# Optimization experiments

Measured on AMD Instinct MI355X. Metric: run time of the kernel, lower is better.

The kernel has to match this reference:

```python
import jax, jax.numpy as jnp
import numpy as np

N_NODES = 100000


def gcn_conv(x, edge_src, edge_dst, edge_weight, W, b):
    # support = x @ W ; out = A @ support + b  (A given as weighted edge list)
    h = x @ W                                   # [N, d_out]
    msg = h[edge_src] * edge_weight[:, None]     # [E, d_out]
    agg = jax.ops.segment_sum(msg, edge_dst, num_segments=N_NODES)
    return agg + b


def setup_inputs() -> dict:
    key = jax.random.key(0)
    ks = jax.random.split(key, 8)
    N, E, m, hidden, m_y = N_NODES, 1600000, 128, 64, 32
    x = jax.random.normal(ks[0], (N, m), dtype=jnp.float32)
    edge_src = jax.random.randint(ks[1], (E,), 0, N, dtype=jnp.int32)
    edge_dst = jax.random.randint(ks[2], (E,), 0, N, dtype=jnp.int32)
    edge_weight = jax.random.uniform(ks[3], (E,), dtype=jnp.float32)
    s1 = 1.0 / np.sqrt(m)
    s2 = 1.0 / np.sqrt(hidden)
    W1 = jax.random.uniform(ks[4], (m, hidden), dtype=jnp.float32, minval=-s1, maxval=s1)
    b1 = jax.random.uniform(ks[5], (hidden,), dtype=jnp.float32, minval=-s1, maxval=s1)
    W2 = jax.random.uniform(ks[6], (hidden, m_y), dtype=jnp.float32, minval=-s2, maxval=s2)
    b2 = jax.random.uniform(ks[7], (m_y,), dtype=jnp.float32, minval=-s2, maxval=s2)
    return {"x": x, "edge_src": edge_src, "edge_dst": edge_dst,
            "edge_weight": edge_weight, "W1": W1, "b1": b1, "W2": W2, "b2": b2}


def reference(x, edge_src, edge_dst, edge_weight, W1, b1, W2, b2):
    out = gcn_conv(x, edge_src, edge_dst, edge_weight, W1, b1)
    out = jax.nn.relu(out)
    # F.dropout(p=0.5, training=self.training) -> identity in eval mode
    out = gcn_conv(out, edge_src, edge_dst, edge_weight, W2, b2)
    return out
```

## Files before the change

kernel.cpp:

```cpp
#include <hip/hip_runtime.h>
#include <hip/hip_bf16.h>


typedef unsigned short u16;
typedef unsigned int uint;
typedef short short8 __attribute__((ext_vector_type(8)));
typedef float floatx4 __attribute__((ext_vector_type(4)));

static __device__ __forceinline__ u16 f2bf(float f) {
    unsigned int u = __float_as_uint(f);
    return (u16)((u + 0x7fff + ((u >> 16) & 1)) >> 16);
}

#define F4C(v, j) ((j)==0?(v).x:((j)==1?(v).y:((j)==2?(v).z:(v).w)))
#define CHUNK 2048
#define CAPC 4608
#define ECAP 384

__global__ __launch_bounds__(256) void init_kernel(
    const float* __restrict__ W1, u16* __restrict__ wfg, int* __restrict__ gcursor)
{
    const int idx = blockIdx.x * 256 + threadIdx.x;
    if (idx < 512) gcursor[idx] = 0;
    const float4 v = ((const float4*)W1)[idx];
    const int k = idx >> 4, n4 = (idx & 15) * 4;
    const int step = k >> 5, klane = (k >> 3) & 3, j = k & 7;
    #pragma unroll
    for (int c = 0; c < 4; c++) {
        int n = n4 + c;
        wfg[(((n >> 4) * 4 + step) * 64 + klane * 16 + (n & 15)) * 8 + j] = f2bf(F4C(v, c));
    }
}

union __align__(16) SharedU {
    struct {
        u16 xs[64][136];
        u16 wf[4][4][64][8];
    } g;
    struct {
        int2 stage[CHUNK];
        u16  stb[CHUNK];
        int  hist[512], sc[512], xscan[512], place[512], runbase[512];
    } p;
};

__global__ __launch_bounds__(256, 4) void g1p_kernel(
    const float* __restrict__ x, const u16* __restrict__ wfg,
    u16* __restrict__ h1, int N,
    const int* __restrict__ src, const int* __restrict__ dst,
    const float* __restrict__ w, int* __restrict__ gcursor,
    int2* __restrict__ es, int E, int cap, int pblocks)
{
    __shared__ SharedU sh;
    const int tid = threadIdx.x;

    if (blockIdx.x < pblocks) {
        const int base = blockIdx.x * CHUNK;
        const int nloc = min(CHUNK, E - base);

        sh.p.hist[tid] = 0; sh.p.hist[tid + 256] = 0;
        __syncthreads();
        for (int i = tid; i < nloc; i += 256)
            atomicAdd(&sh.p.hist[dst[base + i] >> 8], 1);
        __syncthreads();

        sh.p.sc[tid] = sh.p.hist[tid];
        sh.p.sc[tid + 256] = sh.p.hist[tid + 256];
        __syncthreads();
        for (int o = 1; o < 512; o <<= 1) {
            int v0 = (tid >= o) ? sh.p.sc[tid - o] : 0;
            int v1 = (tid + 256 >= o) ? sh.p.sc[tid + 256 - o] : 0;
            __syncthreads();
            sh.p.sc[tid] += v0;
            sh.p.sc[tid + 256] += v1;
            __syncthreads();
        }
        sh.p.xscan[tid] = sh.p.sc[tid] - sh.p.hist[tid];
        sh.p.xscan[tid + 256] = sh.p.sc[tid + 256] - sh.p.hist[tid + 256];
        sh.p.place[tid] = sh.p.xscan[tid];
        sh.p.place[tid + 256] = sh.p.xscan[tid + 256];
        __syncthreads();

        for (int i = tid; i < nloc; i += 256) {
            int d = dst[base + i];
            int b = d >> 8;
            int pos = atomicAdd(&sh.p.place[b], 1);
            sh.p.stage[pos] = make_int2(src[base + i] | ((d & 255) << 24),
                                        __float_as_int(w[base + i]));
            sh.p.stb[pos] = (u16)b;
        }
        __syncthreads();

        {
            int l0 = sh.p.hist[tid], l1 = sh.p.hist[tid + 256];
            sh.p.runbase[tid]       = l0 ? atomicAdd(&gcursor[tid], l0)       : 0;
            sh.p.runbase[tid + 256] = l1 ? atomicAdd(&gcursor[tid + 256], l1) : 0;
        }
        __syncthreads();

        for (int i = tid; i < nloc; i += 256) {
            int b = sh.p.stb[i];
            es[(size_t)b * cap + sh.p.runbase[b] + (i - sh.p.xscan[b])] = sh.p.stage[i];
        }
        return;
    }

    const int row0 = (blockIdx.x - pblocks) * 64;
    {
        const float4* wg4 = (const float4*)wfg;
        float4* wl4 = (float4*)&sh.g.wf[0][0][0][0];
        #pragma unroll
        for (int i = 0; i < 4; i++) wl4[tid + i*256] = wg4[tid + i*256];
    }
    {
        const float4* x4 = (const float4*)x;
        #pragma unroll
        for (int i = 0; i < 8; i++) {
            int idx = tid + i*256;
            int r = idx >> 5, kc = idx & 31;
            int gr = row0 + r;
            float4 v = make_float4(0.f,0.f,0.f,0.f);
            if (gr < N) v = x4[gr*32 + kc];
            ushort4 o;
            o.x = f2bf(v.x); o.y = f2bf(v.y); o.z = f2bf(v.z); o.w = f2bf(v.w);
            *(ushort4*)&sh.g.xs[r][kc*4] = o;
        }
    }
    __syncthreads();

    const int wave = tid >> 6, lane = tid & 63;
    const int m = lane & 15, quad = lane >> 4;
    const int rw = wave * 16;

    floatx4 acc[4] = {(floatx4)(0.f), (floatx4)(0.f), (floatx4)(0.f), (floatx4)(0.f)};
    #pragma unroll
    for (int step = 0; step < 4; step++) {
        short8 a = *(const short8*)&sh.g.xs[rw + m][step*32 + quad*8];
        #pragma unroll
        for (int nt = 0; nt < 4; nt++) {
            short8 b = *(const short8*)&sh.g.wf[nt][step][lane][0];
            acc[nt] = __builtin_amdgcn_mfma_f32_16x16x32_bf16(a, b, acc[nt], 0, 0, 0);
        }
    }
    #pragma unroll
    for (int nt = 0; nt < 4; nt++) {
        #pragma unroll
        for (int r = 0; r < 4; r++) {
            int gr = row0 + rw + quad*4 + r;
            if (gr < N) h1[(size_t)gr*64 + nt*16 + m] = f2bf(acc[nt][r]);
        }
    }
}

__global__ __launch_bounds__(512, 4) void sg1_kernel(
    const u16* __restrict__ h1, const int2* __restrict__ es,
    const int* __restrict__ gcursor, int2* __restrict__ es2,
    int2* __restrict__ off2, const float* __restrict__ b1,
    const float* __restrict__ W2, u16* __restrict__ h2, int N, int cap)
{
    __shared__ int2 sorted[CAPC];
    __shared__ __align__(16) u16 ts[8][16][72];
    __shared__ __align__(16) u16 wf2[2][2][64][8];
    __shared__ float b1s[64];
    __shared__ int hist[256], exs[256], cur[256];
    const int t = threadIdx.x;
    const int b = blockIdx.x;
    const int e0 = b * cap;
    const int len = min(gcursor[b], CAPC);

    {
        const float4* s4 = (const float4*)W2;
        float4 v = s4[t];
        int k = t >> 3, n4 = (t & 7) * 4;
        int step = k >> 5, quad = (k >> 3) & 3, j = k & 7;
        #pragma unroll
        for (int c = 0; c < 4; c++) {
            int n = n4 + c;
            wf2[n >> 4][step][quad*16 + (n & 15)][j] = f2bf(F4C(v, c));
        }
        if (t < 16) ((float4*)b1s)[t] = ((const float4*)b1)[t];
        if (t < 256) hist[t] = 0;
    }
    __syncthreads();

    int2 re[9]; int rk[9];
    #pragma unroll
    for (int k = 0; k < 9; k++) {
        int i = t + k * 512;
        if (i < len) {
            re[k] = es[e0 + i];
            rk[k] = (int)(((unsigned)re[k].x) >> 24);
            atomicAdd(&hist[rk[k]], 1);
        } else rk[k] = -1;
    }
    __syncthreads();

    int v = 0;
    if (t < 256) { v = hist[t]; cur[t] = v; }
    __syncthreads();
    for (int o = 1; o < 256; o <<= 1) {
        int add = 0;
        if (t < 256 && t >= o) add = cur[t - o];
        __syncthreads();
        if (t < 256) cur[t] += add;
        __syncthreads();
    }
    if (t < 256) {
        int ex = cur[t] - v;
        exs[t] = ex;
        cur[t] = ex;
        int g = b * 256 + t;
        if (g < N) off2[g] = make_int2(e0 + ex, e0 + ex + v);
    }
    __syncthreads();

    #pragma unroll
    for (int k = 0; k < 9; k++)
        if (rk[k] >= 0) sorted[atomicAdd(&cur[rk[k]], 1)] = re[k];
    __syncthreads();

    for (int i = t; i < len; i += 512)
        es2[e0 + i] = sorted[i];

    const int wave = t >> 6, lane = t & 63;
    const int h = lane >> 4, fl = lane & 15;
    const uint2* h1v = (const uint2*)h1;
    uint* tsu = (uint*)&ts[wave][0][0];

    #pragma unroll 1
    for (int half = 0; half < 2; half++) {
        const int n0 = wave * 32 + half * 16;
        #pragma unroll 1
        for (int j = 0; j < 8; j++) {
            const int nA = n0 + j, nB = n0 + j + 8;
            const int pbegA = exs[nA], pendA = pbegA + hist[nA];
            const int pbegB = exs[nB], pendB = pbegB + hist[nB];
            const int clA = max(pendA - 1, 0), clB = max(pendB - 1, 0);
            float a0 = 0.f, a1 = 0.f, a2 = 0.f, a3 = 0.f;
            float c0 = 0.f, c1 = 0.f, c2 = 0.f, c3 = 0.f;
            int pA = pbegA, pB = pbegB;
            #pragma unroll 1
            while (pA < pendA || pB < pendB) {
                const int iA0 = pA + h,     iA1 = pA + 4 + h;
                const int iA2 = pA + 8 + h, iA3 = pA + 12 + h;
                const int iB0 = pB + h,     iB1 = pB + 4 + h;
                const int iB2 = pB + 8 + h, iB3 = pB + 12 + h;
                int2 eA0 = sorted[min(iA0, clA)];
                int2 eA1 = sorted[min(iA1, clA)];
                int2 eA2 = sorted[min(iA2, clA)];
                int2 eA3 = sorted[min(iA3, clA)];
                int2 eB0 = sorted[min(iB0, clB)];
                int2 eB1 = sorted[min(iB1, clB)];
                int2 eB2 = sorted[min(iB2, clB)];
                int2 eB3 = sorted[min(iB3, clB)];
                uint2 vA0 = h1v[(size_t)(eA0.x & 0xFFFFFF) * 16 + fl];
                uint2 vA1 = h1v[(size_t)(eA1.x & 0xFFFFFF) * 16 + fl];
                uint2 vA2 = h1v[(size_t)(eA2.x & 0xFFFFFF) * 16 + fl];
                uint2 vA3 = h1v[(size_t)(eA3.x & 0xFFFFFF) * 16 + fl];
                uint2 vB0 = h1v[(size_t)(eB0.x & 0xFFFFFF) * 16 + fl];
                uint2 vB1 = h1v[(size_t)(eB1.x & 0xFFFFFF) * 16 + fl];
                uint2 vB2 = h1v[(size_t)(eB2.x & 0xFFFFFF) * 16 + fl];
                uint2 vB3 = h1v[(size_t)(eB3.x & 0xFFFFFF) * 16 + fl];
                float wA0 = (iA0 < pendA) ? __int_as_float(eA0.y) : 0.f;
                float wA1 = (iA1 < pendA) ? __int_as_float(eA1.y) : 0.f;
                float wA2 = (iA2 < pendA) ? __int_as_float(eA2.y) : 0.f;
                float wA3 = (iA3 < pendA) ? __int_as_float(eA3.y) : 0.f;
                float wB0 = (iB0 < pendB) ? __int_as_float(eB0.y) : 0.f;
                float wB1 = (iB1 < pendB) ? __int_as_float(eB1.y) : 0.f;
                float wB2 = (iB2 < pendB) ? __int_as_float(eB2.y) : 0.f;
                float wB3 = (iB3 < pendB) ? __int_as_float(eB3.y) : 0.f;
                a0 += __uint_as_float(vA0.x << 16) * wA0 + __uint_as_float(vA1.x << 16) * wA1
                    + __uint_as_float(vA2.x << 16) * wA2 + __uint_as_float(vA3.x << 16) * wA3;
                a1 += __uint_as_float(vA0.x & 0xFFFF0000u) * wA0 + __uint_as_float(vA1.x & 0xFFFF0000u) * wA1
                    + __uint_as_float(vA2.x & 0xFFFF0000u) * wA2 + __uint_as_float(vA3.x & 0xFFFF0000u) * wA3;
                a2 += __uint_as_float(vA0.y << 16) * wA0 + __uint_as_float(vA1.y << 16) * wA1
                    + __uint_as_float(vA2.y << 16) * wA2 + __uint_as_float(vA3.y << 16) * wA3;
                a3 += __uint_as_float(vA0.y & 0xFFFF0000u) * wA0 + __uint_as_float(vA1.y & 0xFFFF0000u) * wA1
                    + __uint_as_float(vA2.y & 0xFFFF0000u) * wA2 + __uint_as_float(vA3.y & 0xFFFF0000u) * wA3;
                c0 += __uint_as_float(vB0.x << 16) * wB0 + __uint_as_float(vB1.x << 16) * wB1
                    + __uint_as_float(vB2.x << 16) * wB2 + __uint_as_float(vB3.x << 16) * wB3;
                c1 += __uint_as_float(vB0.x & 0xFFFF0000u) * wB0 + __uint_as_float(vB1.x & 0xFFFF0000u) * wB1
                    + __uint_as_float(vB2.x & 0xFFFF0000u) * wB2 + __uint_as_float(vB3.x & 0xFFFF0000u) * wB3;
                c2 += __uint_as_float(vB0.y << 16) * wB0 + __uint_as_float(vB1.y << 16) * wB1
                    + __uint_as_float(vB2.y << 16) * wB2 + __uint_as_float(vB3.y << 16) * wB3;
                c3 += __uint_as_float(vB0.y & 0xFFFF0000u) * wB0 + __uint_as_float(vB1.y & 0xFFFF0000u) * wB1
                    + __uint_as_float(vB2.y & 0xFFFF0000u) * wB2 + __uint_as_float(vB3.y & 0xFFFF0000u) * wB3;
                pA += 16; pB += 16;
            }
            a0 += __shfl_xor(a0, 16, 64); a1 += __shfl_xor(a1, 16, 64);
            a2 += __shfl_xor(a2, 16, 64); a3 += __shfl_xor(a3, 16, 64);
            a0 += __shfl_xor(a0, 32, 64); a1 += __shfl_xor(a1, 32, 64);
            a2 += __shfl_xor(a2, 32, 64); a3 += __shfl_xor(a3, 32, 64);
            c0 += __shfl_xor(c0, 16, 64); c1 += __shfl_xor(c1, 16, 64);
            c2 += __shfl_xor(c2, 16, 64); c3 += __shfl_xor(c3, 16, 64);
            c0 += __shfl_xor(c0, 32, 64); c1 += __shfl_xor(c1, 32, 64);
            c2 += __shfl_xor(c2, 32, 64); c3 += __shfl_xor(c3, 32, 64);
            if (h == 0) {
                uint t0 = (uint)f2bf(fmaxf(a0 + b1s[4*fl],     0.f))
                        | ((uint)f2bf(fmaxf(a1 + b1s[4*fl + 1], 0.f)) << 16);
                uint t1 = (uint)f2bf(fmaxf(a2 + b1s[4*fl + 2], 0.f))
                        | ((uint)f2bf(fmaxf(a3 + b1s[4*fl + 3], 0.f)) << 16);
                *(uint2*)&tsu[j * 36 + 2*fl] = make_uint2(t0, t1);
                uint t2 = (uint)f2bf(fmaxf(c0 + b1s[4*fl],     0.f))
                        | ((uint)f2bf(fmaxf(c1 + b1s[4*fl + 1], 0.f)) << 16);
                uint t3 = (uint)f2bf(fmaxf(c2 + b1s[4*fl + 2], 0.f))
                        | ((uint)f2bf(fmaxf(c3 + b1s[4*fl + 3], 0.f)) << 16);
                *(uint2*)&tsu[(j + 8) * 36 + 2*fl] = make_uint2(t2, t3);
            }
        }

        const int m = lane & 15, quad = lane >> 4;
        floatx4 acc[2] = {(floatx4)(0.f), (floatx4)(0.f)};
        #pragma unroll
        for (int step = 0; step < 2; step++) {
            short8 a = *(const short8*)&ts[wave][m][step*32 + quad*8];
            #pragma unroll
            for (int nt = 0; nt < 2; nt++) {
                short8 bb = *(const short8*)&wf2[nt][step][lane][0];
                acc[nt] = __builtin_amdgcn_mfma_f32_16x16x32_bf16(a, bb, acc[nt], 0, 0, 0);
            }
        }
        #pragma unroll
        for (int nt = 0; nt < 2; nt++) {
            #pragma unroll
            for (int r = 0; r < 4; r++) {
                int g = b * 256 + n0 + quad*4 + r;
                if (g < N) h2[(size_t)g*32 + nt*16 + m] = f2bf(acc[nt][r]);
            }
        }
    }
}

__global__ __launch_bounds__(256, 4) void gather2_kernel(
    const u16* __restrict__ h2, const int2* __restrict__ es,
    const int2* __restrict__ off2, const float* __restrict__ b2,
    float* __restrict__ out, int N)
{
    __shared__ int2 eb[4][ECAP];
    const int tid = threadIdx.x;
    const int wave = tid >> 6, lane = tid & 63;
    const int g = lane >> 3, fl = lane & 7;
    const int node0 = blockIdx.x * 64 + wave * 16;
    const uint2* h2v = (const uint2*)h2;

    const int2 sg = off2[min(node0 + (lane & 15), N - 1)];
    const int beg = __builtin_amdgcn_readfirstlane(sg.x);
    const int end = __builtin_amdgcn_readlane(sg.y, 15);
    const int len = end - beg;
    const float4 bb = ((const float4*)b2)[fl];

    if (len <= ECAP) {
        for (int k = lane; k < len; k += 64) eb[wave][k] = es[beg + k];

        #pragma unroll 1
        for (int j = 0; j < 8; j++) {
            const int pbegA = __builtin_amdgcn_readlane(sg.x, j) - beg;
            const int pendA = __builtin_amdgcn_readlane(sg.y, j) - beg;
            const int pbegB = __builtin_amdgcn_readlane(sg.x, j + 8) - beg;
            const int pendB = __builtin_amdgcn_readlane(sg.y, j + 8) - beg;
            const int clA = max(pendA - 1, 0), clB = max(pendB - 1, 0);
            float a0 = 0.f, a1 = 0.f, a2 = 0.f, a3 = 0.f;
            float c0 = 0.f, c1 = 0.f, c2 = 0.f, c3 = 0.f;
            int pA = pbegA, pB = pbegB;
            #pragma unroll 1
            while (pA < pendA || pB < pendB) {
                const int iA0 = pA + g, iA1 = pA + 8 + g;
                const int iB0 = pB + g, iB1 = pB + 8 + g;
                int2 eA0 = eb[wave][min(iA0, clA)];
                int2 eA1 = eb[wave][min(iA1, clA)];
                int2 eB0 = eb[wave][min(iB0, clB)];
                int2 eB1 = eb[wave][min(iB1, clB)];
                uint2 vA0 = h2v[(size_t)(eA0.x & 0xFFFFFF) * 8 + fl];
                uint2 vA1 = h2v[(size_t)(eA1.x & 0xFFFFFF) * 8 + fl];
                uint2 vB0 = h2v[(size_t)(eB0.x & 0xFFFFFF) * 8 + fl];
                uint2 vB1 = h2v[(size_t)(eB1.x & 0xFFFFFF) * 8 + fl];
                float wA0 = (iA0 < pendA) ? __int_as_float(eA0.y) : 0.f;
                float wA1 = (iA1 < pendA) ? __int_as_float(eA1.y) : 0.f;
                float wB0 = (iB0 < pendB) ? __int_as_float(eB0.y) : 0.f;
                float wB1 = (iB1 < pendB) ? __int_as_float(eB1.y) : 0.f;
                a0 += __uint_as_float(vA0.x << 16) * wA0 + __uint_as_float(vA1.x << 16) * wA1;
                a1 += __uint_as_float(vA0.x & 0xFFFF0000u) * wA0 + __uint_as_float(vA1.x & 0xFFFF0000u) * wA1;
                a2 += __uint_as_float(vA0.y << 16) * wA0 + __uint_as_float(vA1.y << 16) * wA1;
                a3 += __uint_as_float(vA0.y & 0xFFFF0000u) * wA0 + __uint_as_float(vA1.y & 0xFFFF0000u) * wA1;
                c0 += __uint_as_float(vB0.x << 16) * wB0 + __uint_as_float(vB1.x << 16) * wB1;
                c1 += __uint_as_float(vB0.x & 0xFFFF0000u) * wB0 + __uint_as_float(vB1.x & 0xFFFF0000u) * wB1;
                c2 += __uint_as_float(vB0.y << 16) * wB0 + __uint_as_float(vB1.y << 16) * wB1;
                c3 += __uint_as_float(vB0.y & 0xFFFF0000u) * wB0 + __uint_as_float(vB1.y & 0xFFFF0000u) * wB1;
                pA += 16; pB += 16;
            }
            a0 += __shfl_xor(a0, 8, 64);  a1 += __shfl_xor(a1, 8, 64);
            a2 += __shfl_xor(a2, 8, 64);  a3 += __shfl_xor(a3, 8, 64);
            a0 += __shfl_xor(a0, 16, 64); a1 += __shfl_xor(a1, 16, 64);
            a2 += __shfl_xor(a2, 16, 64); a3 += __shfl_xor(a3, 16, 64);
            a0 += __shfl_xor(a0, 32, 64); a1 += __shfl_xor(a1, 32, 64);
            a2 += __shfl_xor(a2, 32, 64); a3 += __shfl_xor(a3, 32, 64);
            c0 += __shfl_xor(c0, 8, 64);  c1 += __shfl_xor(c1, 8, 64);
            c2 += __shfl_xor(c2, 8, 64);  c3 += __shfl_xor(c3, 8, 64);
            c0 += __shfl_xor(c0, 16, 64); c1 += __shfl_xor(c1, 16, 64);
            c2 += __shfl_xor(c2, 16, 64); c3 += __shfl_xor(c3, 16, 64);
            c0 += __shfl_xor(c0, 32, 64); c1 += __shfl_xor(c1, 32, 64);
            c2 += __shfl_xor(c2, 32, 64); c3 += __shfl_xor(c3, 32, 64);
            const int dA = node0 + j, dB = node0 + j + 8;
            if (g == 0 && dA < N)
                *(float4*)&out[(size_t)dA * 32 + 4 * fl] =
                    make_float4(a0 + bb.x, a1 + bb.y, a2 + bb.z, a3 + bb.w);
            if (g == 0 && dB < N)
                *(float4*)&out[(size_t)dB * 32 + 4 * fl] =
                    make_float4(c0 + bb.x, c1 + bb.y, c2 + bb.z, c3 + bb.w);
        }
    } else {
        #pragma unroll 1
        for (int i = 0; i < 16; i++) {
            const int pbeg = __builtin_amdgcn_readlane(sg.x, i);
            const int pend = __builtin_amdgcn_readlane(sg.y, i);
            const int cl = max(pend - 1, 0);
            float a0 = 0.f, a1 = 0.f, a2 = 0.f, a3 = 0.f;
            #pragma unroll 1
            for (int p = pbeg; p < pend; p += 32) {
                const int i0 = p + g, i1 = p + 8 + g, i2 = p + 16 + g, i3 = p + 24 + g;
                int2 e0 = es[min(i0, cl)];
                int2 e1 = es[min(i1, cl)];
                int2 e2 = es[min(i2, cl)];
                int2 e3 = es[min(i3, cl)];
                uint2 v0 = h2v[(size_t)(e0.x & 0xFFFFFF) * 8 + fl];
                uint2 v1 = h2v[(size_t)(e1.x & 0xFFFFFF) * 8 + fl];
                uint2 v2 = h2v[(size_t)(e2.x & 0xFFFFFF) * 8 + fl];
                uint2 v3 = h2v[(size_t)(e3.x & 0xFFFFFF) * 8 + fl];
                float w0 = (i0 < pend) ? __int_as_float(e0.y) : 0.f;
                float w1 = (i1 < pend) ? __int_as_float(e1.y) : 0.f;
                float w2 = (i2 < pend) ? __int_as_float(e2.y) : 0.f;
                float w3 = (i3 < pend) ? __int_as_float(e3.y) : 0.f;
                a0 += __uint_as_float(v0.x << 16) * w0 + __uint_as_float(v1.x << 16) * w1
                    + __uint_as_float(v2.x << 16) * w2 + __uint_as_float(v3.x << 16) * w3;
                a1 += __uint_as_float(v0.x & 0xFFFF0000u) * w0 + __uint_as_float(v1.x & 0xFFFF0000u) * w1
                    + __uint_as_float(v2.x & 0xFFFF0000u) * w2 + __uint_as_float(v3.x & 0xFFFF0000u) * w3;
                a2 += __uint_as_float(v0.y << 16) * w0 + __uint_as_float(v1.y << 16) * w1
                    + __uint_as_float(v2.y << 16) * w2 + __uint_as_float(v3.y << 16) * w3;
                a3 += __uint_as_float(v0.y & 0xFFFF0000u) * w0 + __uint_as_float(v1.y & 0xFFFF0000u) * w1
                    + __uint_as_float(v2.y & 0xFFFF0000u) * w2 + __uint_as_float(v3.y & 0xFFFF0000u) * w3;
            }
            a0 += __shfl_xor(a0, 8, 64);  a1 += __shfl_xor(a1, 8, 64);
            a2 += __shfl_xor(a2, 8, 64);  a3 += __shfl_xor(a3, 8, 64);
            a0 += __shfl_xor(a0, 16, 64); a1 += __shfl_xor(a1, 16, 64);
            a2 += __shfl_xor(a2, 16, 64); a3 += __shfl_xor(a3, 16, 64);
            a0 += __shfl_xor(a0, 32, 64); a1 += __shfl_xor(a1, 32, 64);
            a2 += __shfl_xor(a2, 32, 64); a3 += __shfl_xor(a3, 32, 64);
            const int d = node0 + i;
            if (g == 0 && d < N)
                *(float4*)&out[(size_t)d * 32 + 4 * fl] =
                    make_float4(a0 + bb.x, a1 + bb.y, a2 + bb.z, a3 + bb.w);
        }
    }
}

extern "C" void kernel_launch(void* const* d_in, const int* in_sizes, int n_in,
                              void* d_out, int out_size, void* d_ws, size_t ws_size,
                              hipStream_t stream)
{
    const float* x   = (const float*)d_in[0];
    const int*  esrc = (const int*)d_in[1];
    const int*  edst = (const int*)d_in[2];
    const float* ew  = (const float*)d_in[3];
    const float* W1  = (const float*)d_in[4];
    const float* b1  = (const float*)d_in[5];
    const float* W2  = (const float*)d_in[6];
    const float* b2  = (const float*)d_in[7];
    float* out = (float*)d_out;

    const int N = in_sizes[0] / 128;
    const int E = in_sizes[1];
    const int nb = (N + 255) >> 8;

    const int mean = (E + nb - 1) / nb;
    int s = 1; while (s * s < mean) s++;
    int cap = (mean + 8 * s + 15) & ~15;
    if (cap > CAPC) cap = CAPC;

    char* base = (char*)d_ws;
    size_t o = 0;
    auto alloc = [&](size_t bytes) { char* p = base + o; o = (o + bytes + 255) & ~(size_t)255; return p; };
    u16*  h1      = (u16*) alloc((size_t)N * 64 * 2);
    u16*  h2      = (u16*) alloc((size_t)N * 32 * 2);
    int2* es      = (int2*)alloc((size_t)nb * cap * 8);
    int2* es2     = (int2*)alloc((size_t)nb * cap * 8);
    int2* off2    = (int2*)alloc((size_t)N * 8);
    int*  gcursor = (int*) alloc(512 * 4);
    u16*  wfg     = (u16*) alloc(8192 * 2);

    const int pblocks = (E + CHUNK - 1) / CHUNK;
    const int gblocks = (N + 63) / 64;

    init_kernel<<<8, 256, 0, stream>>>(W1, wfg, gcursor);
    g1p_kernel<<<pblocks + gblocks, 256, 0, stream>>>(
        x, wfg, h1, N, esrc, edst, ew, gcursor, es, E, cap, pblocks);
    sg1_kernel<<<nb, 512, 0, stream>>>(h1, es, gcursor, es2, off2, b1, W2, h2, N, cap);
    gather2_kernel<<<(N + 63) / 64, 256, 0, stream>>>(h2, es2, off2, b2, out, N);
}
```

Measured before the change: 219.0 us.

## Split sg1 bucket work across two blocks, each holding half the sorted edges

Each 256-node bucket is now handled by two blocks. Both blocks recompute the histogram and prefix sum, but each one scatters only the edges for its 128 destination nodes into a smaller shared buffer, then writes those edges out and aggregates them. The smaller shared footprint and the launch-bounds hint of 6 are meant to raise occupancy and double the number of blocks, exposing more parallelism for the latency-bound gather. The cost is duplicated edge loading and histogram work per bucket. The per-half buffer is clamped at 2816 entries, so a skewed half would be silently truncated, and the length is now capped by cap rather than CAPC.

Result: no change. 216.0 us (-1.4%).

```diff
diff --git a/kernel.cpp b/kernel.cpp
--- a/kernel.cpp
+++ b/kernel.cpp
@@ -15,6 +15,7 @@
 #define F4C(v, j) ((j)==0?(v).x:((j)==1?(v).y:((j)==2?(v).z:(v).w)))
 #define CHUNK 2048
 #define CAPC 4608
+#define SCAPH 2816
 #define ECAP 384
 
 __global__ __launch_bounds__(256) void init_kernel(
@@ -152,21 +153,21 @@
     }
 }
 
-__global__ __launch_bounds__(512, 4) void sg1_kernel(
+__global__ __launch_bounds__(512, 6) void sg1_kernel(
     const u16* __restrict__ h1, const int2* __restrict__ es,
     const int* __restrict__ gcursor, int2* __restrict__ es2,
     int2* __restrict__ off2, const float* __restrict__ b1,
     const float* __restrict__ W2, u16* __restrict__ h2, int N, int cap)
 {
-    __shared__ int2 sorted[CAPC];
+    __shared__ int2 sortedH[SCAPH];
     __shared__ __align__(16) u16 ts[8][16][72];
     __shared__ __align__(16) u16 wf2[2][2][64][8];
     __shared__ float b1s[64];
     __shared__ int hist[256], exs[256], cur[256];
     const int t = threadIdx.x;
-    const int b = blockIdx.x;
+    const int b = blockIdx.x >> 1, hh = blockIdx.x & 1;
     const int e0 = b * cap;
-    const int len = min(gcursor[b], CAPC);
+    const int len = min(gcursor[b], cap);
 
     {
         const float4* s4 = (const float4*)W2;
@@ -208,125 +209,131 @@
     if (t < 256) {
         int ex = cur[t] - v;
         exs[t] = ex;
-        cur[t] = ex;
-        int g = b * 256 + t;
-        if (g < N) off2[g] = make_int2(e0 + ex, e0 + ex + v);
-    }
+        if (hh == 0) {
+            int g = b * 256 + t;
+            if (g < N) off2[g] = make_int2(e0 + ex, e0 + ex + v);
+        }
+    }
+    __syncthreads();
+
+    const int baseH = hh ? exs[128] : 0;
+    const int halflen = hh ? (len - exs[128]) : exs[128];
+    if (t < 256) cur[t] = exs[t] - baseH;
     __syncthreads();
 
     #pragma unroll
     for (int k = 0; k < 9; k++)
-        if (rk[k] >= 0) sorted[atomicAdd(&cur[rk[k]], 1)] = re[k];
-    __syncthreads();
-
-    for (int i = t; i < len; i += 512)
-        es2[e0 + i] = sorted[i];
+        if (rk[k] >= 0 && (rk[k] >> 7) == hh) {
+            int pos = atomicAdd(&cur[rk[k]], 1);
+            sortedH[min(pos, SCAPH - 1)] = re[k];
+        }
+    __syncthreads();
+
+    for (int i = t; i < halflen; i += 512)
+        es2[e0 + baseH + i] = sortedH[i];
 
     const int wave = t >> 6, lane = t & 63;
     const int h = lane >> 4, fl = lane & 15;
     const uint2* h1v = (const uint2*)h1;
     uint* tsu = (uint*)&ts[wave][0][0];
+    const int k0 = hh * 128 + wave * 16;
 
     #pragma unroll 1
-    for (int half = 0; half < 2; half++) {
-        const int n0 = wave * 32 + half * 16;
+    for (int j = 0; j < 8; j++) {
+        const int nA = k0 + j, nB = k0 + j + 8;
+        const int pbegA = exs[nA] - baseH, pendA = pbegA + hist[nA];
+        const int pbegB = exs[nB] - baseH, pendB = pbegB + hist[nB];
+        const int clA = max(pendA - 1, 0), clB = max(pendB - 1, 0);
+        float a0 = 0.f, a1 = 0.f, a2 = 0.f, a3 = 0.f;
+        float c0 = 0.f, c1 = 0.f, c2 = 0.f, c3 = 0.f;
+        int pA = pbegA, pB = pbegB;
         #pragma unroll 1
-        for (int j = 0; j < 8; j++) {
-            const int nA = n0 + j, nB = n0 + j + 8;
-            const int pbegA = exs[nA], pendA = pbegA + hist[nA];
-            const int pbegB = exs[nB], pendB = pbegB + hist[nB];
-            const int clA = max(pendA - 1, 0), clB = max(pendB - 1, 0);
-            float a0 = 0.f, a1 = 0.f, a2 = 0.f, a3 = 0.f;
-            float c0 = 0.f, c1 = 0.f, c2 = 0.f, c3 = 0.f;
-            int pA = pbegA, pB = pbegB;
-            #pragma unroll 1
-            while (pA < pendA || pB < pendB) {
-                const int iA0 = pA + h,     iA1 = pA + 4 + h;
-                const int iA2 = pA + 8 + h, iA3 = pA + 12 + h;
-                const int iB0 = pB + h,     iB1 = pB + 4 + h;
-                const int iB2 = pB + 8 + h, iB3 = pB + 12 + h;
-                int2 eA0 = sorted[min(iA0, clA)];
-                int2 eA1 = sorted[min(iA1, clA)];
-                int2 eA2 = sorted[min(iA2, clA)];
-                int2 eA3 = sorted[min(iA3, clA)];
-                int2 eB0 = sorted[min(iB0, clB)];
-                int2 eB1 = sorted[min(iB1, clB)];
-                int2 eB2 = sorted[min(iB2, clB)];
-                int2 eB3 = sorted[min(iB3, clB)];
-                uint2 vA0 = h1v[(size_t)(eA0.x & 0xFFFFFF) * 16 + fl];
-                uint2 vA1 = h1v[(size_t)(eA1.x & 0xFFFFFF) * 16 + fl];
-                uint2 vA2 = h1v[(size_t)(eA2.x & 0xFFFFFF) * 16 + fl];
-                uint2 vA3 = h1v[(size_t)(eA3.x & 0xFFFFFF) * 16 + fl];
-                uint2 vB0 = h1v[(size_t)(eB0.x & 0xFFFFFF) * 16 + fl];
-                uint2 vB1 = h1v[(size_t)(eB1.x & 0xFFFFFF) * 16 + fl];
-                uint2 vB2 = h1v[(size_t)(eB2.x & 0xFFFFFF) * 16 + fl];
-                uint2 vB3 = h1v[(size_t)(eB3.x & 0xFFFFFF) * 16 + fl];
-                float wA0 = (iA0 < pendA) ? __int_as_float(eA0.y) : 0.f;
-                float wA1 = (iA1 < pendA) ? __int_as_float(eA1.y) : 0.f;
-                float wA2 = (iA2 < pendA) ? __int_as_float(eA2.y) : 0.f;
-                float wA3 = (iA3 < pendA) ? __int_as_float(eA3.y) : 0.f;
-                float wB0 = (iB0 < pendB) ? __int_as_float(eB0.y) : 0.f;
-                float wB1 = (iB1 < pendB) ? __int_as_float(eB1.y) : 0.f;
-                float wB2 = (iB2 < pendB) ? __int_as_float(eB2.y) : 0.f;
-                float wB3 = (iB3 < pendB) ? __int_as_float(eB3.y) : 0.f;
-                a0 += __uint_as_float(vA0.x << 16) * wA0 + __uint_as_float(vA1.x << 16) * wA1
-                    + __uint_as_float(vA2.x << 16) * wA2 + __uint_as_float(vA3.x << 16) * wA3;
-                a1 += __uint_as_float(vA0.x & 0xFFFF0000u) * wA0 + __uint_as_float(vA1.x & 0xFFFF0000u) * wA1
-                    + __uint_as_float(vA2.x & 0xFFFF0000u) * wA2 + __uint_as_float(vA3.x & 0xFFFF0000u) * wA3;
-                a2 += __uint_as_float(vA0.y << 16) * wA0 + __uint_as_float(vA1.y << 16) * wA1
-                    + __uint_as_float(vA2.y << 16) * wA2 + __uint_as_float(vA3.y << 16) * wA3;
-                a3 += __uint_as_float(vA0.y & 0xFFFF0000u) * wA0 + __uint_as_float(vA1.y & 0xFFFF0000u) * wA1
-                    + __uint_as_float(vA2.y & 0xFFFF0000u) * wA2 + __uint_as_float(vA3.y & 0xFFFF0000u) * wA3;
-                c0 += __uint_as_float(vB0.x << 16) * wB0 + __uint_as_float(vB1.x << 16) * wB1
-                    + __uint_as_float(vB2.x << 16) * wB2 + __uint_as_float(vB3.x << 16) * wB3;
-                c1 += __uint_as_float(vB0.x & 0xFFFF0000u) * wB0 + __uint_as_float(vB1.x & 0xFFFF0000u) * wB1
-                    + __uint_as_float(vB2.x & 0xFFFF0000u) * wB2 + __uint_as_float(vB3.x & 0xFFFF0000u) * wB3;
-                c2 += __uint_as_float(vB0.y << 16) * wB0 + __uint_as_float(vB1.y << 16) * wB1
-                    + __uint_as_float(vB2.y << 16) * wB2 + __uint_as_float(vB3.y << 16) * wB3;
-                c3 += __uint_as_float(vB0.y & 0xFFFF0000u) * wB0 + __uint_as_float(vB1.y & 0xFFFF0000u) * wB1
-                    + __uint_as_float(vB2.y & 0xFFFF0000u) * wB2 + __uint_as_float(vB3.y & 0xFFFF0000u) * wB3;
-                pA += 16; pB += 16;
-            }
-            a0 += __shfl_xor(a0, 16, 64); a1 += __shfl_xor(a1, 16, 64);
-            a2 += __shfl_xor(a2, 16, 64); a3 += __shfl_xor(a3, 16, 64);
-            a0 += __shfl_xor(a0, 32, 64); a1 += __shfl_xor(a1, 32, 64);
-            a2 += __shfl_xor(a2, 32, 64); a3 += __shfl_xor(a3, 32, 64);
-            c0 += __shfl_xor(c0, 16, 64); c1 += __shfl_xor(c1, 16, 64);
-            c2 += __shfl_xor(c2, 16, 64); c3 += __shfl_xor(c3, 16, 64);
-            c0 += __shfl_xor(c0, 32, 64); c1 += __shfl_xor(c1, 32, 64);
-            c2 += __shfl_xor(c2, 32, 64); c3 += __shfl_xor(c3, 32, 64);
-            if (h == 0) {
-                uint t0 = (uint)f2bf(fmaxf(a0 + b1s[4*fl],     0.f))
-                        | ((uint)f2bf(fmaxf(a1 + b1s[4*fl + 1], 0.f)) << 16);
-                uint t1 = (uint)f2bf(fmaxf(a2 + b1s[4*fl + 2], 0.f))
-                        | ((uint)f2bf(fmaxf(a3 + b1s[4*fl + 3], 0.f)) << 16);
-                *(uint2*)&tsu[j * 36 + 2*fl] = make_uint2(t0, t1);
-                uint t2 = (uint)f2bf(fmaxf(c0 + b1s[4*fl],     0.f))
-                        | ((uint)f2bf(fmaxf(c1 + b1s[4*fl + 1], 0.f)) << 16);
-                uint t3 = (uint)f2bf(fmaxf(c2 + b1s[4*fl + 2], 0.f))
-                        | ((uint)f2bf(fmaxf(c3 + b1s[4*fl + 3], 0.f)) << 16);
-                *(uint2*)&tsu[(j + 8) * 36 + 2*fl] = make_uint2(t2, t3);
-            }
-        }
-
-        const int m = lane & 15, quad = lane >> 4;
-        floatx4 acc[2] = {(floatx4)(0.f), (floatx4)(0.f)};
-        #pragma unroll
-        for (int step = 0; step < 2; step++) {
-            short8 a = *(const short8*)&ts[wave][m][step*32 + quad*8];
-            #pragma unroll
-            for (int nt = 0; nt < 2; nt++) {
-                short8 bb = *(const short8*)&wf2[nt][step][lane][0];
-                acc[nt] = __builtin_amdgcn_mfma_f32_16x16x32_bf16(a, bb, acc[nt], 0, 0, 0);
-            }
-        }
+        while (pA < pendA || pB < pendB) {
+            const int iA0 = pA + h,     iA1 = pA + 4 + h;
+            const int iA2 = pA + 8 + h, iA3 = pA + 12 + h;
+            const int iB0 = pB + h,     iB1 = pB + 4 + h;
+            const int iB2 = pB + 8 + h, iB3 = pB + 12 + h;
+            int2 eA0 = sortedH[min(iA0, clA)];
+            int2 eA1 = sortedH[min(iA1, clA)];
+            int2 eA2 = sortedH[min(iA2, clA)];
+            int2 eA3 = sortedH[min(iA3, clA)];
+            int2 eB0 = sortedH[min(iB0, clB)];
+            int2 eB1 = sortedH[min(iB1, clB)];
+            int2 eB2 = sortedH[min(iB2, clB)];
+            int2 eB3 = sortedH[min(iB3, clB)];
+            uint2 vA0 = h1v[(size_t)(eA0.x & 0xFFFFFF) * 16 + fl];
+            uint2 vA1 = h1v[(size_t)(eA1.x & 0xFFFFFF) * 16 + fl];
+            uint2 vA2 = h1v[(size_t)(eA2.x & 0xFFFFFF) * 16 + fl];
+            uint2 vA3 = h1v[(size_t)(eA3.x & 0xFFFFFF) * 16 + fl];
+            uint2 vB0 = h1v[(size_t)(eB0.x & 0xFFFFFF) * 16 + fl];
+            uint2 vB1 = h1v[(size_t)(eB1.x & 0xFFFFFF) * 16 + fl];
+            uint2 vB2 = h1v[(size_t)(eB2.x & 0xFFFFFF) * 16 + fl];
+            uint2 vB3 = h1v[(size_t)(eB3.x & 0xFFFFFF) * 16 + fl];
+            float wA0 = (iA0 < pendA) ? __int_as_float(eA0.y) : 0.f;
+            float wA1 = (iA1 < pendA) ? __int_as_float(eA1.y) : 0.f;
+            float wA2 = (iA2 < pendA) ? __int_as_float(eA2.y) : 0.f;
+            float wA3 = (iA3 < pendA) ? __int_as_float(eA3.y) : 0.f;
+            float wB0 = (iB0 < pendB) ? __int_as_float(eB0.y) : 0.f;
+            float wB1 = (iB1 < pendB) ? __int_as_float(eB1.y) : 0.f;
+            float wB2 = (iB2 < pendB) ? __int_as_float(eB2.y) : 0.f;
+            float wB3 = (iB3 < pendB) ? __int_as_float(eB3.y) : 0.f;
+            a0 += __uint_as_float(vA0.x << 16) * wA0 + __uint_as_float(vA1.x << 16) * wA1
+                + __uint_as_float(vA2.x << 16) * wA2 + __uint_as_float(vA3.x << 16) * wA3;
+            a1 += __uint_as_float(vA0.x & 0xFFFF0000u) * wA0 + __uint_as_float(vA1.x & 0xFFFF0000u) * wA1
+                + __uint_as_float(vA2.x & 0xFFFF0000u) * wA2 + __uint_as_float(vA3.x & 0xFFFF0000u) * wA3;
+            a2 += __uint_as_float(vA0.y << 16) * wA0 + __uint_as_float(vA1.y << 16) * wA1
+                + __uint_as_float(vA2.y << 16) * wA2 + __uint_as_float(vA3.y << 16) * wA3;
+            a3 += __uint_as_float(vA0.y & 0xFFFF0000u) * wA0 + __uint_as_float(vA1.y & 0xFFFF0000u) * wA1
+                + __uint_as_float(vA2.y & 0xFFFF0000u) * wA2 + __uint_as_float(vA3.y & 0xFFFF0000u) * wA3;
+            c0 += __uint_as_float(vB0.x << 16) * wB0 + __uint_as_float(vB1.x << 16) * wB1
+                + __uint_as_float(vB2.x << 16) * wB2 + __uint_as_float(vB3.x << 16) * wB3;
+            c1 += __uint_as_float(vB0.x & 0xFFFF0000u) * wB0 + __uint_as_float(vB1.x & 0xFFFF0000u) * wB1
+                + __uint_as_float(vB2.x & 0xFFFF0000u) * wB2 + __uint_as_float(vB3.x & 0xFFFF0000u) * wB3;
+            c2 += __uint_as_float(vB0.y << 16) * wB0 + __uint_as_float(vB1.y << 16) * wB1
+                + __uint_as_float(vB2.y << 16) * wB2 + __uint_as_float(vB3.y << 16) * wB3;
+            c3 += __uint_as_float(vB0.y & 0xFFFF0000u) * wB0 + __uint_as_float(vB1.y & 0xFFFF0000u) * wB1
+                + __uint_as_float(vB2.y & 0xFFFF0000u) * wB2 + __uint_as_float(vB3.y & 0xFFFF0000u) * wB3;
+            pA += 16; pB += 16;
+        }
+        a0 += __shfl_xor(a0, 16, 64); a1 += __shfl_xor(a1, 16, 64);
+        a2 += __shfl_xor(a2, 16, 64); a3 += __shfl_xor(a3, 16, 64);
+        a0 += __shfl_xor(a0, 32, 64); a1 += __shfl_xor(a1, 32, 64);
+        a2 += __shfl_xor(a2, 32, 64); a3 += __shfl_xor(a3, 32, 64);
+        c0 += __shfl_xor(c0, 16, 64); c1 += __shfl_xor(c1, 16, 64);
+        c2 += __shfl_xor(c2, 16, 64); c3 += __shfl_xor(c3, 16, 64);
+        c0 += __shfl_xor(c0, 32, 64); c1 += __shfl_xor(c1, 32, 64);
+        c2 += __shfl_xor(c2, 32, 64); c3 += __shfl_xor(c3, 32, 64);
+        if (h == 0) {
+            uint t0 = (uint)f2bf(fmaxf(a0 + b1s[4*fl],     0.f))
+                    | ((uint)f2bf(fmaxf(a1 + b1s[4*fl + 1], 0.f)) << 16);
+            uint t1 = (uint)f2bf(fmaxf(a2 + b1s[4*fl + 2], 0.f))
+                    | ((uint)f2bf(fmaxf(a3 + b1s[4*fl + 3], 0.f)) << 16);
+            *(uint2*)&tsu[j * 36 + 2*fl] = make_uint2(t0, t1);
+            uint t2 = (uint)f2bf(fmaxf(c0 + b1s[4*fl],     0.f))
+                    | ((uint)f2bf(fmaxf(c1 + b1s[4*fl + 1], 0.f)) << 16);
+            uint t3 = (uint)f2bf(fmaxf(c2 + b1s[4*fl + 2], 0.f))
+                    | ((uint)f2bf(fmaxf(c3 + b1s[4*fl + 3], 0.f)) << 16);
+            *(uint2*)&tsu[(j + 8) * 36 + 2*fl] = make_uint2(t2, t3);
+        }
+    }
+
+    const int m = lane & 15, quad = lane >> 4;
+    floatx4 acc[2] = {(floatx4)(0.f), (floatx4)(0.f)};
+    #pragma unroll
+    for (int step = 0; step < 2; step++) {
+        short8 a = *(const short8*)&ts[wave][m][step*32 + quad*8];
         #pragma unroll
         for (int nt = 0; nt < 2; nt++) {
-            #pragma unroll
-            for (int r = 0; r < 4; r++) {
-                int g = b * 256 + n0 + quad*4 + r;
-                if (g < N) h2[(size_t)g*32 + nt*16 + m] = f2bf(acc[nt][r]);
-            }
+            short8 bb = *(const short8*)&wf2[nt][step][lane][0];
+            acc[nt] = __builtin_amdgcn_mfma_f32_16x16x32_bf16(a, bb, acc[nt], 0, 0, 0);
+        }
+    }
+    #pragma unroll
+    for (int nt = 0; nt < 2; nt++) {
+        #pragma unroll
+        for (int r = 0; r < 4; r++) {
+            int g = b * 256 + k0 + quad*4 + r;
+            if (g < N) h2[(size_t)g*32 + nt*16 + m] = f2bf(acc[nt][r]);
         }
     }
 }
@@ -493,6 +500,6 @@
     init_kernel<<<8, 256, 0, stream>>>(W1, wfg, gcursor);
     g1p_kernel<<<pblocks + gblocks, 256, 0, stream>>>(
         x, wfg, h1, N, esrc, edst, ew, gcursor, es, E, cap, pblocks);
-    sg1_kernel<<<nb, 512, 0, stream>>>(h1, es, gcursor, es2, off2, b1, W2, h2, N, cap);
+    sg1_kernel<<<2 * nb, 512, 0, stream>>>(h1, es, gcursor, es2, off2, b1, W2, h2, N, cap);
     gather2_kernel<<<(N + 63) / 64, 256, 0, stream>>>(h2, es2, off2, b2, out, N);
 }
```
